# Kernel optimization log

Measured on AMD Instinct MI355X. Metric: run time of the kernel, lower is better.

Reference implementation:

```python
import jax, jax.numpy as jnp
import numpy as np

TEMPERATURE = 0.1


def setup_inputs() -> dict:
    key = jax.random.key(0)
    k1, k2 = jax.random.split(key)
    B, B_pos, D = 8192, 8192, 1024
    generated = jax.random.normal(k1, (B, D), dtype=jnp.float32)
    positive = jax.random.normal(k2, (B_pos, D), dtype=jnp.float32)
    return {"generated": generated, "positive": positive}


def _pairwise_dist_sq(x, y):
    # (N, M) squared L2 distances, clamped at 0
    x_norm = jnp.sum(x * x, axis=-1, keepdims=True)          # (N, 1)
    y_norm = jnp.sum(y * y, axis=-1, keepdims=True)          # (M, 1)
    d2 = x_norm + y_norm.T - 2.0 * (x @ y.T)
    return jnp.clip(d2, 0.0)


def reference(generated, positive):
    gen = generated.reshape(generated.shape[0], -1)
    pos = positive.reshape(positive.shape[0], -1)
    B = gen.shape[0]

    # Attraction: softmax over distances to positives.
    dist_pos = jnp.sqrt(_pairwise_dist_sq(gen, pos))          # (B, B_pos)
    w_pos = jax.nn.softmax(-dist_pos / TEMPERATURE, axis=1)
    # sum_j w_ij (pos_j - gen_i) == (w_pos @ pos) - gen  (rows of w sum to 1)
    attraction = w_pos @ pos - gen                            # (B, D)

    # Repulsion: softmax over distances to other generated samples (diag masked).
    d2_neg = _pairwise_dist_sq(gen, gen)
    eye = jnp.eye(B, dtype=bool)
    dist_neg = jnp.sqrt(jnp.where(eye, jnp.inf, d2_neg))      # inf diag -> weight 0
    w_neg = jax.nn.softmax(-dist_neg / TEMPERATURE, axis=1)
    repulsion = w_neg @ gen - gen                             # (B, D)

    drift = attraction - repulsion
    target = jax.lax.stop_gradient(gen + drift)
    loss = jnp.mean((gen - target) ** 2)

    drift_norm = jnp.mean(jnp.linalg.norm(drift, axis=-1))
    attraction_norm = jnp.mean(jnp.linalg.norm(attraction, axis=-1))
    repulsion_norm = jnp.mean(jnp.linalg.norm(repulsion, axis=-1))
    return (loss, drift_norm, attraction_norm, repulsion_norm)
```

## Files before the change

kernel.cpp:

```cpp
#include <hip/hip_runtime.h>
#include <stdint.h>

#define INV_T 10.0f
#define SHIFT_ 460.0f
#define MROWS 8192
#define DDIM 1024
#define CHUNK 1024

typedef __attribute__((ext_vector_type(8))) short bf16x8;
typedef __attribute__((ext_vector_type(4))) float f32x4;

__device__ __forceinline__ float bf2f(unsigned short u) {
  return __uint_as_float(((unsigned int)u) << 16);
}
__device__ __forceinline__ unsigned short f2bf(float f) {
  unsigned int u = __float_as_uint(f);
  return (unsigned short)((u + 0x7FFFu + ((u >> 16) & 1u)) >> 16);
}
__device__ __forceinline__ void gl2lds16(const unsigned short* g, unsigned short* l) {
  __builtin_amdgcn_global_load_lds((const __attribute__((address_space(1))) void*)g,
                                   (__attribute__((address_space(3))) void*)l, 16, 0, 0);
}

__global__ void prep_kernel(const float* __restrict__ gen, const float* __restrict__ pos,
                            unsigned short* __restrict__ gen_h, unsigned short* __restrict__ pos_h,
                            float* __restrict__ gn2, float* __restrict__ pn2) {
  int b = blockIdx.x;
  const float* src; unsigned short* dst; float* n2; int row;
  if (b < MROWS) { src = gen; dst = gen_h; n2 = gn2; row = b; }
  else           { src = pos; dst = pos_h; n2 = pn2; row = b - MROWS; }
  int t = threadIdx.x;
  float4 v = ((const float4*)(src + (size_t)row * DDIM))[t];
  float ss = v.x * v.x + v.y * v.y + v.z * v.z + v.w * v.w;
  ushort4 o;
  o.x = f2bf(v.x); o.y = f2bf(v.y); o.z = f2bf(v.z); o.w = f2bf(v.w);
  ((ushort4*)(dst + (size_t)row * DDIM))[t] = o;
#pragma unroll
  for (int m = 1; m < 64; m <<= 1) ss += __shfl_xor(ss, m);
  __shared__ float red[4];
  if ((t & 63) == 0) red[t >> 6] = ss;
  __syncthreads();
  if (t == 0) n2[row] = red[0] + red[1] + red[2] + red[3];
}

__global__ void transpose_kernel(const float* __restrict__ gen, const float* __restrict__ pos,
                                 unsigned short* __restrict__ genT, unsigned short* __restrict__ posT) {
  __shared__ float tile[64][65];
  int b = blockIdx.x;
  const float* src; unsigned short* dst;
  if (b < 2048) { src = gen; dst = genT; }
  else          { src = pos; dst = posT; b -= 2048; }
  int tj = b >> 4, td = b & 15;
  int t = threadIdx.x;
#pragma unroll
  for (int it = 0; it < 16; ++it) {
    int idx = it * 256 + t;
    int r = idx >> 6, c = idx & 63;
    tile[r][c] = src[(size_t)(tj * 64 + r) * DDIM + td * 64 + c];
  }
  __syncthreads();
#pragma unroll
  for (int it = 0; it < 16; ++it) {
    int idx = it * 256 + t;
    int d = idx >> 6, j = idx & 63;
    dst[(size_t)(td * 64 + d) * MROWS + tj * 64 + j] = f2bf(tile[j][d]);
  }
}

__launch_bounds__(256, 2)
__global__ void gemm_sc(const unsigned short* __restrict__ Aq,
                        const unsigned short* __restrict__ Bka,
                        const unsigned short* __restrict__ Bkr,
                        unsigned short* __restrict__ Pa, unsigned short* __restrict__ Pr,
                        int j0,
                        const float* __restrict__ gn2, const float* __restrict__ pn2,
                        float* __restrict__ lsumA, float* __restrict__ lsumR) {
  __shared__ __align__(16) unsigned short Al[128 * 64];
  __shared__ __align__(16) unsigned short Bal[128 * 64];
  __shared__ __align__(16) unsigned short Brl[128 * 64];

  const int orig = blockIdx.x + 64 * blockIdx.y;
  const int wid = (orig & 7) * 64 + (orig >> 3);
  const int by = wid & 7;
  const int bx = wid >> 3;

  const int t = threadIdx.x;
  const int w = t >> 6, lane = t & 63, l15 = lane & 15, quad = lane >> 4;
  const int wm = w >> 1, wn = w & 1;
  const long m0 = (long)bx * 128;
  const long n0 = (long)by * 128;
  const int trow = t >> 3;
  const int tcol = (((t & 7) ^ (trow & 7)) * 8);

  f32x4 accA[4][4], accR[4][4];
#pragma unroll
  for (int i = 0; i < 4; ++i)
#pragma unroll
    for (int j = 0; j < 4; ++j) {
      accA[i][j] = (f32x4){0.f, 0.f, 0.f, 0.f};
      accR[i][j] = (f32x4){0.f, 0.f, 0.f, 0.f};
    }

  const unsigned short* Ab  = Aq  + (m0 + trow) * DDIM + tcol;
  const unsigned short* Bab = Bka + (n0 + trow) * DDIM + tcol;
  const unsigned short* Brb = Bkr + (n0 + trow) * DDIM + tcol;
  unsigned short* Alw = Al  + t * 8;
  unsigned short* Baw = Bal + t * 8;
  unsigned short* Brw = Brl + t * 8;
  const int ue = (quad ^ (l15 & 7)) * 8;

  for (int ks = 0; ks < DDIM / 64; ++ks) {
    const long ko = (long)ks * 64;
#pragma unroll
    for (int i = 0; i < 4; ++i) gl2lds16(Ab + (long)i * 32 * DDIM + ko, Alw + i * 2048);
#pragma unroll
    for (int i = 0; i < 4; ++i) gl2lds16(Bab + (long)i * 32 * DDIM + ko, Baw + i * 2048);
#pragma unroll
    for (int i = 0; i < 4; ++i) gl2lds16(Brb + (long)i * 32 * DDIM + ko, Brw + i * 2048);
    __syncthreads();
#pragma unroll
    for (int kk = 0; kk < 2; ++kk) {
      const int uo = ue ^ (kk * 32);
      bf16x8 af[4], ba[4], br[4];
#pragma unroll
      for (int mi = 0; mi < 4; ++mi)
        af[mi] = *(const bf16x8*)(Al + (wm * 64 + mi * 16 + l15) * 64 + uo);
#pragma unroll
      for (int ni = 0; ni < 4; ++ni) {
        ba[ni] = *(const bf16x8*)(Bal + (wn * 64 + ni * 16 + l15) * 64 + uo);
        br[ni] = *(const bf16x8*)(Brl + (wn * 64 + ni * 16 + l15) * 64 + uo);
      }
#pragma unroll
      for (int mi = 0; mi < 4; ++mi)
#pragma unroll
        for (int ni = 0; ni < 4; ++ni) {
          accA[mi][ni] = __builtin_amdgcn_mfma_f32_16x16x32_bf16(af[mi], ba[ni], accA[mi][ni], 0, 0, 0);
          accR[mi][ni] = __builtin_amdgcn_mfma_f32_16x16x32_bf16(af[mi], br[ni], accR[mi][ni], 0, 0, 0);
        }
    }
    __syncthreads();
  }

#pragma unroll
  for (int mi = 0; mi < 4; ++mi) {
    float rs[4] = {0.f, 0.f, 0.f, 0.f};
#pragma unroll
    for (int ni = 0; ni < 4; ++ni) {
      int c = (int)n0 + wn * 64 + ni * 16 + l15;
      float kn = pn2[j0 + c];
#pragma unroll
      for (int reg = 0; reg < 4; ++reg) {
        long r = m0 + wm * 64 + mi * 16 + quad * 4 + reg;
        float v = accA[mi][ni][reg];
        float d2 = gn2[r] + kn - 2.0f * v;
        float p = __expf(SHIFT_ - INV_T * sqrtf(fmaxf(d2, 0.0f)));
        rs[reg] += p;
        Pa[r * (long)CHUNK + c] = f2bf(p);
      }
    }
#pragma unroll
    for (int reg = 0; reg < 4; ++reg) {
      float v = rs[reg];
      v += __shfl_xor(v, 1); v += __shfl_xor(v, 2);
      v += __shfl_xor(v, 4); v += __shfl_xor(v, 8);
      if (l15 == 0) atomicAdd(&lsumA[m0 + wm * 64 + mi * 16 + quad * 4 + reg], v);
    }
  }
#pragma unroll
  for (int mi = 0; mi < 4; ++mi) {
    float rs[4] = {0.f, 0.f, 0.f, 0.f};
#pragma unroll
    for (int ni = 0; ni < 4; ++ni) {
      int c = (int)n0 + wn * 64 + ni * 16 + l15;
      float kn = gn2[j0 + c];
#pragma unroll
      for (int reg = 0; reg < 4; ++reg) {
        long r = m0 + wm * 64 + mi * 16 + quad * 4 + reg;
        float v = accR[mi][ni][reg];
        float d2 = gn2[r] + kn - 2.0f * v;
        float p = __expf(SHIFT_ - INV_T * sqrtf(fmaxf(d2, 0.0f)));
        if ((int)r == (j0 + c)) p = 0.0f;
        rs[reg] += p;
        Pr[r * (long)CHUNK + c] = f2bf(p);
      }
    }
#pragma unroll
    for (int reg = 0; reg < 4; ++reg) {
      float v = rs[reg];
      v += __shfl_xor(v, 1); v += __shfl_xor(v, 2);
      v += __shfl_xor(v, 4); v += __shfl_xor(v, 8);
      if (l15 == 0) atomicAdd(&lsumR[m0 + wm * 64 + mi * 16 + quad * 4 + reg], v);
    }
  }
}

#define KSEG(Abase, Bbase, LDA_, LDB_)                                                     \
  {                                                                                        \
    const unsigned short* Ab_ = (Abase) + (m0 + trow) * (LDA_) + tcol;                     \
    const unsigned short* Bb_ = (Bbase) + (n0 + trow) * (LDB_) + tcol;                     \
    for (int ks = 0; ks < 16; ++ks) {                                                      \
      const long ko = (long)ks * 64;                                                       \
      _Pragma("unroll")                                                                    \
      for (int i = 0; i < 4; ++i) gl2lds16(Ab_ + (long)i * 32 * (LDA_) + ko, Alw + i * 2048); \
      _Pragma("unroll")                                                                    \
      for (int i = 0; i < 4; ++i) gl2lds16(Bb_ + (long)i * 32 * (LDB_) + ko, Blw + i * 2048); \
      __syncthreads();                                                                     \
      _Pragma("unroll")                                                                    \
      for (int kk = 0; kk < 2; ++kk) {                                                     \
        const int uo = ue ^ (kk * 32);                                                     \
        bf16x8 af[4], bfr[4];                                                              \
        _Pragma("unroll")                                                                  \
        for (int mi = 0; mi < 4; ++mi)                                                     \
          af[mi] = *(const bf16x8*)(Al + (wm * 64 + mi * 16 + l15) * 64 + uo);             \
        _Pragma("unroll")                                                                  \
        for (int ni = 0; ni < 4; ++ni)                                                     \
          bfr[ni] = *(const bf16x8*)(Bl + (wn * 64 + ni * 16 + l15) * 64 + uo);            \
        _Pragma("unroll")                                                                  \
        for (int mi = 0; mi < 4; ++mi)                                                     \
          _Pragma("unroll")                                                                \
          for (int ni = 0; ni < 4; ++ni)                                                   \
            acc[mi][ni] = __builtin_amdgcn_mfma_f32_16x16x32_bf16(af[mi], bfr[ni], acc[mi][ni], 0, 0, 0); \
      }                                                                                    \
      __syncthreads();                                                                     \
    }                                                                                      \
  }

__launch_bounds__(256, 2)
__global__ void gemm_pv(const unsigned short* __restrict__ Pa0, const unsigned short* __restrict__ Pr0,
                        const unsigned short* __restrict__ Pa1, const unsigned short* __restrict__ Pr1,
                        const unsigned short* __restrict__ Va0, const unsigned short* __restrict__ Vr0,
                        const unsigned short* __restrict__ Va1, const unsigned short* __restrict__ Vr1,
                        unsigned short* __restrict__ OA, unsigned short* __restrict__ OR_,
                        int first) {
  __shared__ __align__(16) unsigned short Al[128 * 64];
  __shared__ __align__(16) unsigned short Bl[128 * 64];

  const int orig = blockIdx.x + 64 * (blockIdx.y + 8 * blockIdx.z);
  const int wid = (orig & 7) * 128 + (orig >> 3);
  const int by = wid & 7;
  const int bx = (wid >> 3) & 63;
  const int z = wid >> 9;

  const unsigned short* A0 = z ? Pr0 : Pa0;
  const unsigned short* B0 = z ? Vr0 : Va0;
  const unsigned short* A1 = z ? Pr1 : Pa1;
  const unsigned short* B1 = z ? Vr1 : Va1;

  const int t = threadIdx.x;
  const int w = t >> 6, lane = t & 63, l15 = lane & 15, quad = lane >> 4;
  const int wm = w >> 1, wn = w & 1;
  const long m0 = (long)bx * 128;
  const long n0 = (long)by * 128;
  const int trow = t >> 3;
  const int tcol = (((t & 7) ^ (trow & 7)) * 8);

  f32x4 acc[4][4];
#pragma unroll
  for (int i = 0; i < 4; ++i)
#pragma unroll
    for (int j = 0; j < 4; ++j) acc[i][j] = (f32x4){0.f, 0.f, 0.f, 0.f};

  unsigned short* Alw = Al + t * 8;
  unsigned short* Blw = Bl + t * 8;
  const int ue = (quad ^ (l15 & 7)) * 8;

  KSEG(A0, B0, CHUNK, MROWS);
  KSEG(A1, B1, CHUNK, MROWS);

  unsigned short* Oh = z ? OR_ : OA;
#pragma unroll
  for (int mi = 0; mi < 4; ++mi)
#pragma unroll
    for (int ni = 0; ni < 4; ++ni) {
      long c = n0 + wn * 64 + ni * 16 + l15;
#pragma unroll
      for (int reg = 0; reg < 4; ++reg) {
        long r = m0 + wm * 64 + mi * 16 + quad * 4 + reg;
        long off = r * DDIM + c;
        float v = acc[mi][ni][reg];
        Oh[off] = f2bf(first ? v : (bf2f(Oh[off]) + v));
      }
    }
}
#undef KSEG

__global__ void epi_kernel(const unsigned short* __restrict__ OA, const unsigned short* __restrict__ OR_,
                           const float* __restrict__ lsumA, const float* __restrict__ lsumR,
                           const float* __restrict__ genf, float* __restrict__ gs) {
  __shared__ float wsL[4], wsD[4], wsA[4], wsR[4];
  const int t = threadIdx.x;
  const int w = t >> 6;
  const int lane = t & 63;
  float accL = 0.f, accD = 0.f, accA = 0.f, accR = 0.f;

  for (int i = 0; i < 8; ++i) {
    const int row = blockIdx.x * 32 + w * 8 + i;
    const float invlA = 1.0f / lsumA[row];
    const float invlR = 1.0f / lsumR[row];
    float ssA = 0.f, ssR = 0.f, ssD = 0.f;
#pragma unroll
    for (int u = 0; u < 4; ++u) {
      const long off = (long)row * DDIM + u * 256 + lane * 4;
      float4 g = *(const float4*)(genf + off);
      ushort4 oa = *(const ushort4*)(OA + off);
      ushort4 orr = *(const ushort4*)(OR_ + off);
      float g4[4] = {g.x, g.y, g.z, g.w};
      float a4[4] = {bf2f(oa.x), bf2f(oa.y), bf2f(oa.z), bf2f(oa.w)};
      float r4[4] = {bf2f(orr.x), bf2f(orr.y), bf2f(orr.z), bf2f(orr.w)};
#pragma unroll
      for (int e = 0; e < 4; ++e) {
        float a_ = a4[e] * invlA - g4[e];
        float r_ = r4[e] * invlR - g4[e];
        float d_ = a_ - r_;
        ssA += a_ * a_; ssR += r_ * r_; ssD += d_ * d_;
      }
    }
#pragma unroll
    for (int m = 1; m < 64; m <<= 1) {
      ssA += __shfl_xor(ssA, m);
      ssR += __shfl_xor(ssR, m);
      ssD += __shfl_xor(ssD, m);
    }
    accA += sqrtf(ssA); accR += sqrtf(ssR); accD += sqrtf(ssD); accL += ssD;
  }
  if (lane == 0) { wsL[w] = accL; wsD[w] = accD; wsA[w] = accA; wsR[w] = accR; }
  __syncthreads();
  if (t == 0) {
    atomicAdd(&gs[0], wsL[0] + wsL[1] + wsL[2] + wsL[3]);
    atomicAdd(&gs[1], wsD[0] + wsD[1] + wsD[2] + wsD[3]);
    atomicAdd(&gs[2], wsA[0] + wsA[1] + wsA[2] + wsA[3]);
    atomicAdd(&gs[3], wsR[0] + wsR[1] + wsR[2] + wsR[3]);
  }
}

__global__ void finalize_kernel(const float* __restrict__ gs, float* __restrict__ out) {
  int t = threadIdx.x;
  if (t == 0) out[0] = gs[0] / (8192.0f * 1024.0f);
  if (t == 1) out[1] = gs[1] / 8192.0f;
  if (t == 2) out[2] = gs[2] / 8192.0f;
  if (t == 3) out[3] = gs[3] / 8192.0f;
}

extern "C" void kernel_launch(void* const* d_in, const int* in_sizes, int n_in,
                              void* d_out, int out_size, void* d_ws, size_t ws_size,
                              hipStream_t stream) {
  const float* gen = (const float*)d_in[0];
  const float* pos = (const float*)d_in[1];
  char* ws = (char*)d_ws;
  const size_t MB = (size_t)1 << 20;
  unsigned short* gen_h = (unsigned short*)(ws + 0 * MB);
  unsigned short* pos_h = (unsigned short*)(ws + 16 * MB);
  unsigned short* genT  = (unsigned short*)(ws + 32 * MB);
  unsigned short* posT  = (unsigned short*)(ws + 48 * MB);
  unsigned short* Pa0   = (unsigned short*)(ws + 64 * MB);
  unsigned short* Pr0   = (unsigned short*)(ws + 80 * MB);
  unsigned short* Pa1   = (unsigned short*)(ws + 96 * MB);
  unsigned short* Pr1   = (unsigned short*)(ws + 112 * MB);
  unsigned short* OhA   = (unsigned short*)(ws + 128 * MB);
  unsigned short* OhR   = (unsigned short*)(ws + 144 * MB);
  float* gn2   = (float*)(ws + 160 * MB);
  float* pn2   = (float*)(ws + 160 * MB + 32768);
  float* lsumA = (float*)(ws + 160 * MB + 65536);
  float* lsumR = (float*)(ws + 160 * MB + 98304);
  float* gs    = (float*)(ws + 160 * MB + 131072);

  hipMemsetAsync(gs, 0, 4 * sizeof(float), stream);
  hipMemsetAsync(lsumA, 0, 2 * MROWS * sizeof(float), stream);
  prep_kernel<<<dim3(16384), dim3(256), 0, stream>>>(gen, pos, gen_h, pos_h, gn2, pn2);
  transpose_kernel<<<dim3(4096), dim3(256), 0, stream>>>(gen, pos, genT, posT);

  for (int p = 0; p < 4; ++p) {
    const int j00 = (2 * p) * CHUNK, j01 = (2 * p + 1) * CHUNK;
    gemm_sc<<<dim3(64, 8), dim3(256), 0, stream>>>(
        gen_h, pos_h + (long)j00 * DDIM, gen_h + (long)j00 * DDIM,
        Pa0, Pr0, j00, gn2, pn2, lsumA, lsumR);
    gemm_sc<<<dim3(64, 8), dim3(256), 0, stream>>>(
        gen_h, pos_h + (long)j01 * DDIM, gen_h + (long)j01 * DDIM,
        Pa1, Pr1, j01, gn2, pn2, lsumA, lsumR);
    gemm_pv<<<dim3(64, 8, 2), dim3(256), 0, stream>>>(
        Pa0, Pr0, Pa1, Pr1,
        posT + j00, genT + j00, posT + j01, genT + j01,
        OhA, OhR, p == 0);
  }

  epi_kernel<<<dim3(256), dim3(256), 0, stream>>>(OhA, OhR, lsumA, lsumR, gen, gs);
  finalize_kernel<<<dim3(1), dim3(64), 0, stream>>>(gs, (float*)d_out);
}
```

Baseline: 814.2 us.

## Split score GEMM into per-branch blocks and batch four chunks per PV pass

The score kernel no longer computes the attraction and repulsion products in one block with two accumulator sets. It now launches a z-dimension of 2, so each block computes a single 128x128 product with half the LDS and accumulator registers. With enough workspace, four 1024-column chunks of probabilities are buffered before each PV GEMM, which then accumulates over four K segments. This halves the read-modify-write passes over the bf16 output accumulators. The cost is that the shared A tile is loaded twice across the split blocks, and the workspace must be larger.

After: 803.1 us. Within noise of the previous version (-1.4%).

```diff
diff --git a/kernel.cpp b/kernel.cpp
--- a/kernel.cpp
+++ b/kernel.cpp
@@ -67,23 +67,34 @@
   }
 }
 
+template <int EPI>
 __launch_bounds__(256, 2)
-__global__ void gemm_sc(const unsigned short* __restrict__ Aq,
-                        const unsigned short* __restrict__ Bka,
-                        const unsigned short* __restrict__ Bkr,
-                        unsigned short* __restrict__ Pa, unsigned short* __restrict__ Pr,
-                        int j0,
-                        const float* __restrict__ gn2, const float* __restrict__ pn2,
-                        float* __restrict__ lsumA, float* __restrict__ lsumR) {
+__global__ void gemm_bt(const unsigned short* __restrict__ A0, const unsigned short* __restrict__ A1,
+                        long lda,
+                        const unsigned short* __restrict__ B0, const unsigned short* __restrict__ B1,
+                        long ldb, int ksteps,
+                        unsigned short* __restrict__ P0, unsigned short* __restrict__ P1,
+                        int pld, int j0,
+                        const float* __restrict__ qn2,
+                        const float* __restrict__ kn2a, const float* __restrict__ kn2b,
+                        float* __restrict__ lsum0, float* __restrict__ lsum1,
+                        unsigned short* __restrict__ O0, unsigned short* __restrict__ O1,
+                        int first) {
   __shared__ __align__(16) unsigned short Al[128 * 64];
-  __shared__ __align__(16) unsigned short Bal[128 * 64];
-  __shared__ __align__(16) unsigned short Brl[128 * 64];
-
-  const int orig = blockIdx.x + 64 * blockIdx.y;
-  const int wid = (orig & 7) * 64 + (orig >> 3);
-  const int by = wid & 7;
-  const int bx = wid >> 3;
-
+  __shared__ __align__(16) unsigned short Bl[128 * 64];
+
+  const int NXB = gridDim.x, NYB = gridDim.y;
+  const int nwg = NXB * NYB * gridDim.z;
+  const int orig = blockIdx.x + NXB * (blockIdx.y + NYB * blockIdx.z);
+  const int wid = (orig & 7) * (nwg >> 3) + (orig >> 3);
+  int bx, by, bz;
+  by = wid % NYB;
+  bx = (wid / NYB) % NXB;
+  bz = wid / (NYB * NXB);
+
+  const int z = bz;
+  const unsigned short* A = z ? A1 : A0;
+  const unsigned short* B = z ? B1 : B0;
   const int t = threadIdx.x;
   const int w = t >> 6, lane = t & 63, l15 = lane & 15, quad = lane >> 4;
   const int wm = w >> 1, wn = w & 1;
@@ -92,105 +103,89 @@
   const int trow = t >> 3;
   const int tcol = (((t & 7) ^ (trow & 7)) * 8);
 
-  f32x4 accA[4][4], accR[4][4];
+  f32x4 acc[4][4];
 #pragma unroll
   for (int i = 0; i < 4; ++i)
 #pragma unroll
-    for (int j = 0; j < 4; ++j) {
-      accA[i][j] = (f32x4){0.f, 0.f, 0.f, 0.f};
-      accR[i][j] = (f32x4){0.f, 0.f, 0.f, 0.f};
-    }
-
-  const unsigned short* Ab  = Aq  + (m0 + trow) * DDIM + tcol;
-  const unsigned short* Bab = Bka + (n0 + trow) * DDIM + tcol;
-  const unsigned short* Brb = Bkr + (n0 + trow) * DDIM + tcol;
-  unsigned short* Alw = Al  + t * 8;
-  unsigned short* Baw = Bal + t * 8;
-  unsigned short* Brw = Brl + t * 8;
+    for (int j = 0; j < 4; ++j) acc[i][j] = (f32x4){0.f, 0.f, 0.f, 0.f};
+
+  const unsigned short* Ab = A + (m0 + trow) * lda + tcol;
+  const unsigned short* Bb = B + (n0 + trow) * ldb + tcol;
+  unsigned short* Alw = Al + t * 8;
+  unsigned short* Blw = Bl + t * 8;
   const int ue = (quad ^ (l15 & 7)) * 8;
 
-  for (int ks = 0; ks < DDIM / 64; ++ks) {
+  for (int ks = 0; ks < ksteps; ++ks) {
     const long ko = (long)ks * 64;
 #pragma unroll
-    for (int i = 0; i < 4; ++i) gl2lds16(Ab + (long)i * 32 * DDIM + ko, Alw + i * 2048);
-#pragma unroll
-    for (int i = 0; i < 4; ++i) gl2lds16(Bab + (long)i * 32 * DDIM + ko, Baw + i * 2048);
-#pragma unroll
-    for (int i = 0; i < 4; ++i) gl2lds16(Brb + (long)i * 32 * DDIM + ko, Brw + i * 2048);
+    for (int i = 0; i < 4; ++i) gl2lds16(Ab + (long)i * 32 * lda + ko, Alw + i * 2048);
+#pragma unroll
+    for (int i = 0; i < 4; ++i) gl2lds16(Bb + (long)i * 32 * ldb + ko, Blw + i * 2048);
     __syncthreads();
 #pragma unroll
     for (int kk = 0; kk < 2; ++kk) {
       const int uo = ue ^ (kk * 32);
-      bf16x8 af[4], ba[4], br[4];
+      bf16x8 af[4], bfr[4];
 #pragma unroll
       for (int mi = 0; mi < 4; ++mi)
         af[mi] = *(const bf16x8*)(Al + (wm * 64 + mi * 16 + l15) * 64 + uo);
 #pragma unroll
+      for (int ni = 0; ni < 4; ++ni)
+        bfr[ni] = *(const bf16x8*)(Bl + (wn * 64 + ni * 16 + l15) * 64 + uo);
+#pragma unroll
+      for (int mi = 0; mi < 4; ++mi)
+#pragma unroll
+        for (int ni = 0; ni < 4; ++ni)
+          acc[mi][ni] = __builtin_amdgcn_mfma_f32_16x16x32_bf16(af[mi], bfr[ni], acc[mi][ni], 0, 0, 0);
+    }
+    __syncthreads();
+  }
+
+  if (EPI == 0) {
+    unsigned short* Pout = z ? P1 : P0;
+    const float* kn2 = z ? kn2b : kn2a;
+    float* lsum = z ? lsum1 : lsum0;
+#pragma unroll
+    for (int mi = 0; mi < 4; ++mi) {
+      float rs[4] = {0.f, 0.f, 0.f, 0.f};
+#pragma unroll
       for (int ni = 0; ni < 4; ++ni) {
-        ba[ni] = *(const bf16x8*)(Bal + (wn * 64 + ni * 16 + l15) * 64 + uo);
-        br[ni] = *(const bf16x8*)(Brl + (wn * 64 + ni * 16 + l15) * 64 + uo);
-      }
-#pragma unroll
-      for (int mi = 0; mi < 4; ++mi)
-#pragma unroll
-        for (int ni = 0; ni < 4; ++ni) {
-          accA[mi][ni] = __builtin_amdgcn_mfma_f32_16x16x32_bf16(af[mi], ba[ni], accA[mi][ni], 0, 0, 0);
-          accR[mi][ni] = __builtin_amdgcn_mfma_f32_16x16x32_bf16(af[mi], br[ni], accR[mi][ni], 0, 0, 0);
+        int c = (int)n0 + wn * 64 + ni * 16 + l15;
+        float kn = kn2[j0 + c];
+#pragma unroll
+        for (int reg = 0; reg < 4; ++reg) {
+          long r = m0 + wm * 64 + mi * 16 + quad * 4 + reg;
+          float v = acc[mi][ni][reg];
+          float d2 = qn2[r] + kn - 2.0f * v;
+          float p = __expf(SHIFT_ - INV_T * sqrtf(fmaxf(d2, 0.0f)));
+          if (z && (int)r == (j0 + c)) p = 0.0f;
+          rs[reg] += p;
+          Pout[r * (long)pld + c] = f2bf(p);
         }
-    }
-    __syncthreads();
-  }
-
-#pragma unroll
-  for (int mi = 0; mi < 4; ++mi) {
-    float rs[4] = {0.f, 0.f, 0.f, 0.f};
-#pragma unroll
-    for (int ni = 0; ni < 4; ++ni) {
-      int c = (int)n0 + wn * 64 + ni * 16 + l15;
-      float kn = pn2[j0 + c];
+      }
 #pragma unroll
       for (int reg = 0; reg < 4; ++reg) {
-        long r = m0 + wm * 64 + mi * 16 + quad * 4 + reg;
-        float v = accA[mi][ni][reg];
-        float d2 = gn2[r] + kn - 2.0f * v;
-        float p = __expf(SHIFT_ - INV_T * sqrtf(fmaxf(d2, 0.0f)));
-        rs[reg] += p;
-        Pa[r * (long)CHUNK + c] = f2bf(p);
-      }
-    }
-#pragma unroll
-    for (int reg = 0; reg < 4; ++reg) {
-      float v = rs[reg];
-      v += __shfl_xor(v, 1); v += __shfl_xor(v, 2);
-      v += __shfl_xor(v, 4); v += __shfl_xor(v, 8);
-      if (l15 == 0) atomicAdd(&lsumA[m0 + wm * 64 + mi * 16 + quad * 4 + reg], v);
-    }
-  }
-#pragma unroll
-  for (int mi = 0; mi < 4; ++mi) {
-    float rs[4] = {0.f, 0.f, 0.f, 0.f};
-#pragma unroll
-    for (int ni = 0; ni < 4; ++ni) {
-      int c = (int)n0 + wn * 64 + ni * 16 + l15;
-      float kn = gn2[j0 + c];
-#pragma unroll
-      for (int reg = 0; reg < 4; ++reg) {
-        long r = m0 + wm * 64 + mi * 16 + quad * 4 + reg;
-        float v = accR[mi][ni][reg];
-        float d2 = gn2[r] + kn - 2.0f * v;
-        float p = __expf(SHIFT_ - INV_T * sqrtf(fmaxf(d2, 0.0f)));
-        if ((int)r == (j0 + c)) p = 0.0f;
-        rs[reg] += p;
-        Pr[r * (long)CHUNK + c] = f2bf(p);
-      }
-    }
-#pragma unroll
-    for (int reg = 0; reg < 4; ++reg) {
-      float v = rs[reg];
-      v += __shfl_xor(v, 1); v += __shfl_xor(v, 2);
-      v += __shfl_xor(v, 4); v += __shfl_xor(v, 8);
-      if (l15 == 0) atomicAdd(&lsumR[m0 + wm * 64 + mi * 16 + quad * 4 + reg], v);
-    }
+        float v = rs[reg];
+        v += __shfl_xor(v, 1); v += __shfl_xor(v, 2);
+        v += __shfl_xor(v, 4); v += __shfl_xor(v, 8);
+        if (l15 == 0) atomicAdd(&lsum[m0 + wm * 64 + mi * 16 + quad * 4 + reg], v);
+      }
+    }
+  } else {
+    unsigned short* Oh = z ? O1 : O0;
+#pragma unroll
+    for (int mi = 0; mi < 4; ++mi)
+#pragma unroll
+      for (int ni = 0; ni < 4; ++ni) {
+        long c = n0 + wn * 64 + ni * 16 + l15;
+#pragma unroll
+        for (int reg = 0; reg < 4; ++reg) {
+          long r = m0 + wm * 64 + mi * 16 + quad * 4 + reg;
+          long off = r * DDIM + c;
+          float v = acc[mi][ni][reg];
+          Oh[off] = f2bf(first ? v : (bf2f(Oh[off]) + v));
+        }
+      }
   }
 }
 
@@ -228,10 +223,14 @@
 __launch_bounds__(256, 2)
 __global__ void gemm_pv(const unsigned short* __restrict__ Pa0, const unsigned short* __restrict__ Pr0,
                         const unsigned short* __restrict__ Pa1, const unsigned short* __restrict__ Pr1,
+                        const unsigned short* __restrict__ Pa2, const unsigned short* __restrict__ Pr2,
+                        const unsigned short* __restrict__ Pa3, const unsigned short* __restrict__ Pr3,
                         const unsigned short* __restrict__ Va0, const unsigned short* __restrict__ Vr0,
                         const unsigned short* __restrict__ Va1, const unsigned short* __restrict__ Vr1,
+                        const unsigned short* __restrict__ Va2, const unsigned short* __restrict__ Vr2,
+                        const unsigned short* __restrict__ Va3, const unsigned short* __restrict__ Vr3,
                         unsigned short* __restrict__ OA, unsigned short* __restrict__ OR_,
-                        int first) {
+                        int first, int nseg) {
   __shared__ __align__(16) unsigned short Al[128 * 64];
   __shared__ __align__(16) unsigned short Bl[128 * 64];
 
@@ -245,6 +244,10 @@
   const unsigned short* B0 = z ? Vr0 : Va0;
   const unsigned short* A1 = z ? Pr1 : Pa1;
   const unsigned short* B1 = z ? Vr1 : Va1;
+  const unsigned short* A2 = z ? Pr2 : Pa2;
+  const unsigned short* B2 = z ? Vr2 : Va2;
+  const unsigned short* A3 = z ? Pr3 : Pa3;
+  const unsigned short* B3 = z ? Vr3 : Va3;
 
   const int t = threadIdx.x;
   const int w = t >> 6, lane = t & 63, l15 = lane & 15, quad = lane >> 4;
@@ -266,6 +269,10 @@
 
   KSEG(A0, B0, CHUNK, MROWS);
   KSEG(A1, B1, CHUNK, MROWS);
+  if (nseg > 2) {
+    KSEG(A2, B2, CHUNK, MROWS);
+    KSEG(A3, B3, CHUNK, MROWS);
+  }
 
   unsigned short* Oh = z ? OR_ : OA;
 #pragma unroll
@@ -348,41 +355,85 @@
   const float* pos = (const float*)d_in[1];
   char* ws = (char*)d_ws;
   const size_t MB = (size_t)1 << 20;
+  const size_t need_quad = 224 * MB + 4 * 32768 + 64;
+
   unsigned short* gen_h = (unsigned short*)(ws + 0 * MB);
   unsigned short* pos_h = (unsigned short*)(ws + 16 * MB);
   unsigned short* genT  = (unsigned short*)(ws + 32 * MB);
   unsigned short* posT  = (unsigned short*)(ws + 48 * MB);
-  unsigned short* Pa0   = (unsigned short*)(ws + 64 * MB);
-  unsigned short* Pr0   = (unsigned short*)(ws + 80 * MB);
-  unsigned short* Pa1   = (unsigned short*)(ws + 96 * MB);
-  unsigned short* Pr1   = (unsigned short*)(ws + 112 * MB);
-  unsigned short* OhA   = (unsigned short*)(ws + 128 * MB);
-  unsigned short* OhR   = (unsigned short*)(ws + 144 * MB);
-  float* gn2   = (float*)(ws + 160 * MB);
-  float* pn2   = (float*)(ws + 160 * MB + 32768);
-  float* lsumA = (float*)(ws + 160 * MB + 65536);
-  float* lsumR = (float*)(ws + 160 * MB + 98304);
-  float* gs    = (float*)(ws + 160 * MB + 131072);
-
-  hipMemsetAsync(gs, 0, 4 * sizeof(float), stream);
-  hipMemsetAsync(lsumA, 0, 2 * MROWS * sizeof(float), stream);
-  prep_kernel<<<dim3(16384), dim3(256), 0, stream>>>(gen, pos, gen_h, pos_h, gn2, pn2);
-  transpose_kernel<<<dim3(4096), dim3(256), 0, stream>>>(gen, pos, genT, posT);
-
-  for (int p = 0; p < 4; ++p) {
-    const int j00 = (2 * p) * CHUNK, j01 = (2 * p + 1) * CHUNK;
-    gemm_sc<<<dim3(64, 8), dim3(256), 0, stream>>>(
-        gen_h, pos_h + (long)j00 * DDIM, gen_h + (long)j00 * DDIM,
-        Pa0, Pr0, j00, gn2, pn2, lsumA, lsumR);
-    gemm_sc<<<dim3(64, 8), dim3(256), 0, stream>>>(
-        gen_h, pos_h + (long)j01 * DDIM, gen_h + (long)j01 * DDIM,
-        Pa1, Pr1, j01, gn2, pn2, lsumA, lsumR);
-    gemm_pv<<<dim3(64, 8, 2), dim3(256), 0, stream>>>(
-        Pa0, Pr0, Pa1, Pr1,
-        posT + j00, genT + j00, posT + j01, genT + j01,
-        OhA, OhR, p == 0);
-  }
-
-  epi_kernel<<<dim3(256), dim3(256), 0, stream>>>(OhA, OhR, lsumA, lsumR, gen, gs);
-  finalize_kernel<<<dim3(1), dim3(64), 0, stream>>>(gs, (float*)d_out);
-}
+
+  if (ws_size >= need_quad) {
+    unsigned short* Pa[4] = {(unsigned short*)(ws + 64 * MB),  (unsigned short*)(ws + 96 * MB),
+                             (unsigned short*)(ws + 128 * MB), (unsigned short*)(ws + 160 * MB)};
+    unsigned short* Pr[4] = {(unsigned short*)(ws + 80 * MB),  (unsigned short*)(ws + 112 * MB),
+                             (unsigned short*)(ws + 144 * MB), (unsigned short*)(ws + 176 * MB)};
+    unsigned short* OhA   = (unsigned short*)(ws + 192 * MB);
+    unsigned short* OhR   = (unsigned short*)(ws + 208 * MB);
+    float* gn2   = (float*)(ws + 224 * MB);
+    float* pn2   = (float*)(ws + 224 * MB + 32768);
+    float* lsumA = (float*)(ws + 224 * MB + 65536);
+    float* lsumR = (float*)(ws + 224 * MB + 98304);
+    float* gs    = (float*)(ws + 224 * MB + 131072);
+
+    hipMemsetAsync(gs, 0, 4 * sizeof(float), stream);
+    hipMemsetAsync(lsumA, 0, 2 * MROWS * sizeof(float), stream);
+    prep_kernel<<<dim3(16384), dim3(256), 0, stream>>>(gen, pos, gen_h, pos_h, gn2, pn2);
+    transpose_kernel<<<dim3(4096), dim3(256), 0, stream>>>(gen, pos, genT, posT);
+
+    for (int p = 0; p < 2; ++p) {
+      for (int q = 0; q < 4; ++q) {
+        const int j0 = (4 * p + q) * CHUNK;
+        gemm_bt<0><<<dim3(64, 8, 2), dim3(256), 0, stream>>>(
+            gen_h, gen_h, DDIM,
+            pos_h + (long)j0 * DDIM, gen_h + (long)j0 * DDIM, DDIM, DDIM / 64,
+            Pa[q], Pr[q], CHUNK, j0, gn2, pn2, gn2, lsumA, lsumR, nullptr, nullptr, 0);
+      }
+      const long j0 = (long)(4 * p) * CHUNK;
+      gemm_pv<<<dim3(64, 8, 2), dim3(256), 0, stream>>>(
+          Pa[0], Pr[0], Pa[1], Pr[1], Pa[2], Pr[2], Pa[3], Pr[3],
+          posT + j0, genT + j0, posT + j0 + CHUNK, genT + j0 + CHUNK,
+          posT + j0 + 2 * CHUNK, genT + j0 + 2 * CHUNK, posT + j0 + 3 * CHUNK, genT + j0 + 3 * CHUNK,
+          OhA, OhR, p == 0, 4);
+    }
+
+    epi_kernel<<<dim3(256), dim3(256), 0, stream>>>(OhA, OhR, lsumA, lsumR, gen, gs);
+    finalize_kernel<<<dim3(1), dim3(64), 0, stream>>>(gs, (float*)d_out);
+  } else {
+    unsigned short* Pa0   = (unsigned short*)(ws + 64 * MB);
+    unsigned short* Pr0   = (unsigned short*)(ws + 80 * MB);
+    unsigned short* Pa1   = (unsigned short*)(ws + 96 * MB);
+    unsigned short* Pr1   = (unsigned short*)(ws + 112 * MB);
+    unsigned short* OhA   = (unsigned short*)(ws + 128 * MB);
+    unsigned short* OhR   = (unsigned short*)(ws + 144 * MB);
+    float* gn2   = (float*)(ws + 160 * MB);
+    float* pn2   = (float*)(ws + 160 * MB + 32768);
+    float* lsumA = (float*)(ws + 160 * MB + 65536);
+    float* lsumR = (float*)(ws + 160 * MB + 98304);
+    float* gs    = (float*)(ws + 160 * MB + 131072);
+
+    hipMemsetAsync(gs, 0, 4 * sizeof(float), stream);
+    hipMemsetAsync(lsumA, 0, 2 * MROWS * sizeof(float), stream);
+    prep_kernel<<<dim3(16384), dim3(256), 0, stream>>>(gen, pos, gen_h, pos_h, gn2, pn2);
+    transpose_kernel<<<dim3(4096), dim3(256), 0, stream>>>(gen, pos, genT, posT);
+
+    for (int p = 0; p < 4; ++p) {
+      const int j00 = (2 * p) * CHUNK, j01 = (2 * p + 1) * CHUNK;
+      gemm_bt<0><<<dim3(64, 8, 2), dim3(256), 0, stream>>>(
+          gen_h, gen_h, DDIM,
+          pos_h + (long)j00 * DDIM, gen_h + (long)j00 * DDIM, DDIM, DDIM / 64,
+          Pa0, Pr0, CHUNK, j00, gn2, pn2, gn2, lsumA, lsumR, nullptr, nullptr, 0);
+      gemm_bt<0><<<dim3(64, 8, 2), dim3(256), 0, stream>>>(
+          gen_h, gen_h, DDIM,
+          pos_h + (long)j01 * DDIM, gen_h + (long)j01 * DDIM, DDIM, DDIM / 64,
+          Pa1, Pr1, CHUNK, j01, gn2, pn2, gn2, lsumA, lsumR, nullptr, nullptr, 0);
+      gemm_pv<<<dim3(64, 8, 2), dim3(256), 0, stream>>>(
+          Pa0, Pr0, Pa1, Pr1, Pa0, Pr0, Pa1, Pr1,
+          posT + (long)j00, genT + (long)j00, posT + (long)j01, genT + (long)j01,
+          posT + (long)j00, genT + (long)j00, posT + (long)j01, genT + (long)j01,
+          OhA, OhR, p == 0, 2);
+    }
+
+    epi_kernel<<<dim3(256), dim3(256), 0, stream>>>(OhA, OhR, lsumA, lsumR, gen, gs);
+    finalize_kernel<<<dim3(1), dim3(64), 0, stream>>>(gs, (float*)d_out);
+  }
+}
```
